# Optimization experiments

Measured on AMD Instinct MI355X. Metric: run time of the kernel, lower is better.

The kernel has to match this reference:

```python
import jax, jax.numpy as jnp
import numpy as np

B, L, H, S = 16, 2048, 1024, 32
P, N_ASP, N_RAT = 256, 8, 5


def _layernorm(x, scale, bias, eps=1e-5):
    mu = jnp.mean(x, axis=-1, keepdims=True)
    var = jnp.mean(jnp.square(x - mu), axis=-1, keepdims=True)
    return (x - mu) * jax.lax.rsqrt(var + eps) * scale + bias


def _bndl(x, ln_s, ln_b, W):
    # BnDropLin eval: LayerNorm -> (Dropout off) -> Linear(no bias)
    return _layernorm(x, ln_s, ln_b) @ W


def setup_inputs() -> dict:
    key = jax.random.key(0)
    ks = jax.random.split(key, 8)
    outputs = jax.random.normal(ks[0], (B, L, H), dtype=jnp.float32)
    mask = jnp.ones((B, L), dtype=jnp.float32)
    # p_index: binary sentence-boundary markers, exactly S per doc, min gap 2
    rng = np.random.default_rng(0)
    p = np.zeros((B, L), dtype=np.int32)
    for b in range(B):
        idx = np.sort(rng.choice(L // 2 - 1, size=S, replace=False)) * 2 + 1
        p[b, idx] = 1
    p_index = jnp.asarray(p)
    sc = 0.02
    params = dict(
        ln_a_s=jnp.ones((H,), jnp.float32), ln_a_b=jnp.zeros((H,), jnp.float32),
        W_a=jax.random.normal(ks[1], (H, P), jnp.float32) * sc,
        ln_s_s=jnp.ones((H,), jnp.float32), ln_s_b=jnp.zeros((H,), jnp.float32),
        W_s=jax.random.normal(ks[2], (H, P), jnp.float32) * sc,
        ln_asp_s=jnp.ones((P,), jnp.float32), ln_asp_b=jnp.zeros((P,), jnp.float32),
        W_asp=jax.random.normal(ks[3], (P, N_ASP + 1), jnp.float32) * sc,
        ln_se_s=jnp.ones((P,), jnp.float32), ln_se_b=jnp.zeros((P,), jnp.float32),
        W_se=jax.random.normal(ks[4], (P, N_RAT), jnp.float32) * sc,
    )
    return dict(outputs=outputs, mask=mask, p_index=p_index, n_sent=S, **params)


def _segment_means(proj, end, start):
    # proj: [B, L, P]; start/end: [B, S] token index ranges [start, end)
    c = jnp.concatenate([jnp.zeros_like(proj[:, :1]), jnp.cumsum(proj, axis=1)], axis=1)  # [B,L+1,P]
    s_end = jnp.take_along_axis(c, end[:, :, None], axis=1)
    s_beg = jnp.take_along_axis(c, start[:, :, None], axis=1)
    cnt = (end - start).astype(proj.dtype)[:, :, None]
    return (s_end - s_beg) / cnt  # [B, S, P]


def reference(outputs, mask, p_index, n_sent,
              ln_a_s, ln_a_b, W_a, ln_s_s, ln_s_b, W_s,
              ln_asp_s, ln_asp_b, W_asp, ln_se_s, ln_se_b, W_se):
    b, l, h = outputs.shape
    n_asp = W_asp.shape[1] - 1
    flat = outputs.reshape(-1, h)
    a_proj = jax.nn.gelu(_bndl(flat, ln_a_s, ln_a_b, W_a), approximate=False).reshape(b, l, -1)
    s_proj = jax.nn.gelu(_bndl(flat, ln_s_s, ln_s_b, W_s), approximate=False).reshape(b, l, -1)
    # sentence boundaries: positions of nonzeros (exactly n_sent per row)
    pos = jnp.where(p_index > 0, jnp.arange(l)[None, :], l)
    pi = jnp.sort(pos, axis=1)[:, :n_sent]                      # [B,S] boundary idx (exclusive end)
    start = jnp.concatenate([jnp.zeros_like(pi[:, :1]), pi[:, :-1] + 1], axis=1)
    a_sent = _segment_means(a_proj, pi, start)                  # [B,S,P]
    s_sent = _segment_means(s_proj, pi, start)                  # [B,S,P]
    a_flat = a_sent.reshape(b * n_sent, -1)
    s_flat = s_sent.reshape(b * n_sent, -1)
    aspect_dist = jax.nn.softmax(_bndl(a_flat, ln_asp_s, ln_asp_b, W_asp), axis=1)  # [N, n_asp+1]
    aw = aspect_dist[:, :n_asp]                                 # [N, n_asp]
    sent_bmm = aw[:, :, None] * s_flat[:, None, :]              # [N, n_asp, P]
    doc_sum = sent_bmm.reshape(b, n_sent, n_asp, -1).sum(axis=1)        # [B, n_asp, P]
    w_sum = aw.reshape(b, n_sent, n_asp).sum(axis=1)[:, :, None]        # [B, n_asp, 1]
    doc_emb = doc_sum / w_sum
    # shared sentiment head (ModuleList([m]*n_asp) aliases one module)
    result = _bndl(doc_emb, ln_se_s, ln_se_b, W_se)             # [B, n_asp, n_rat]
    aspect_doc = aspect_dist.reshape(b, n_sent, n_asp + 1)
    return (result, outputs, aspect_doc)
```

## Files before the change

### kernel.cpp

```cpp
#include <hip/hip_runtime.h>
#include <cstdint>
#include <cstddef>

#define B_   16
#define L_   2048
#define H_   1024
#define S_   32
#define P_   256
#define NASP 8
#define NRAT 5
#define M_   (B_*L_)
#define N_   (2*P_)

typedef unsigned short u16;
typedef __bf16 bf16;
typedef u16  u16x4  __attribute__((ext_vector_type(4)));
typedef u16  u16x8  __attribute__((ext_vector_type(8)));
typedef bf16 bf16x8 __attribute__((ext_vector_type(8)));
typedef float f32x4 __attribute__((ext_vector_type(4)));

__device__ __forceinline__ u16 f2b(float f){
  unsigned int u = __float_as_uint(f);
  u += 0x7FFFu + ((u >> 16) & 1u);
  return (u16)(u >> 16);
}
__device__ __forceinline__ float b2f(u16 v){
  return __uint_as_float(((unsigned int)v) << 16);
}

__device__ __forceinline__ void gload_lds16(const u16* g, u16* l){
  __builtin_amdgcn_global_load_lds(
      (const __attribute__((address_space(1))) unsigned int*)g,
      (__attribute__((address_space(3))) unsigned int*)l, 16, 0, 0);
}

__device__ __forceinline__ float2 block_reduce2(float a, float b){
  __shared__ float sh[8];
  #pragma unroll
  for (int o = 32; o > 0; o >>= 1){
    a += __shfl_down(a, o, 64);
    b += __shfl_down(b, o, 64);
  }
  int w = threadIdx.x >> 6;
  if ((threadIdx.x & 63) == 0){ sh[w] = a; sh[w + 4] = b; }
  __syncthreads();
  float2 r;
  r.x = sh[0] + sh[1] + sh[2] + sh[3];
  r.y = sh[4] + sh[5] + sh[6] + sh[7];
  __syncthreads();
  return r;
}

__global__ void fold_k(const float* __restrict__ Wa, const float* __restrict__ Ws,
                       const float* __restrict__ sa, const float* __restrict__ ba,
                       const float* __restrict__ ss, const float* __restrict__ bs,
                       u16* __restrict__ WcT, float* __restrict__ biasc){
  int n = blockIdx.x;
  const float* W; const float* sc; const float* bi; int col;
  if (n < P_){ W = Wa; sc = sa; bi = ba; col = n; }
  else       { W = Ws; sc = ss; bi = bs; col = n - P_; }
  float bacc = 0.f;
  #pragma unroll
  for (int i = 0; i < 4; ++i){
    int k = threadIdx.x + i * 256;
    float w = W[(size_t)k * P_ + col];
    WcT[(size_t)n * H_ + k] = f2b(w * sc[k]);
    bacc += w * bi[k];
  }
  float2 r = block_reduce2(bacc, 0.f);
  if (threadIdx.x == 0) biasc[n] = r.x;
}

__global__ void markers_k(const int* __restrict__ p_index, int* __restrict__ pi){
  int b = blockIdx.x;
  int lane = threadIdx.x;
  int cnt = 0;
  for (int c = 0; c < L_ / 64; ++c){
    int pos = c * 64 + lane;
    bool f = p_index[(size_t)b * L_ + pos] > 0;
    unsigned long long m = __ballot(f);
    int before = __popcll(m & ((1ull << lane) - 1ull));
    if (f){
      int idx = cnt + before;
      if (idx < S_) pi[b * S_ + idx] = pos;
    }
    cnt += __popcll(m);
  }
}

template<bool FUSE_ECHO>
__global__ void stats_xhat_k(const float* __restrict__ x, u16* __restrict__ xhat,
                             float4* __restrict__ echo){
  int row = blockIdx.x;
  int t = threadIdx.x;
  float4 v = ((const float4*)(x + (size_t)row * H_))[t];
  if (FUSE_ECHO) echo[(size_t)row * (H_ / 4) + t] = v;
  float s  = v.x + v.y + v.z + v.w;
  float ss = v.x*v.x + v.y*v.y + v.z*v.z + v.w*v.w;
  float2 r = block_reduce2(s, ss);
  float mean = r.x * (1.f / H_);
  float var  = fmaxf(r.y * (1.f / H_) - mean * mean, 0.f);
  float rstd = rsqrtf(var + 1e-5f);
  u16x4 o;
  o[0] = f2b((v.x - mean) * rstd);
  o[1] = f2b((v.y - mean) * rstd);
  o[2] = f2b((v.z - mean) * rstd);
  o[3] = f2b((v.w - mean) * rstd);
  ((u16x4*)(xhat + (size_t)row * H_))[t] = o;
}

__global__ __launch_bounds__(256) void gemm_k(const u16* __restrict__ xhat,
                                              const u16* __restrict__ WcT,
                                              const float* __restrict__ biasc,
                                              u16* __restrict__ proj){
  __shared__ __align__(16) u16 As[2 * 128 * 32];
  __shared__ __align__(16) u16 Bs[2 * 128 * 32];
  int t = threadIdx.x;
  unsigned int l = blockIdx.x;
  unsigned int xcd  = l & 7;
  unsigned int slot = l >> 3;
  int nbase = (int)(slot & 3) * 128;
  int mbase = (int)(xcd * 32 + (slot >> 2)) * 128;

  int w = t >> 6, lane = t & 63;
  int wr = w >> 1, wc = w & 1;
  int quad = lane >> 4, l15 = lane & 15;

  int g = (lane & 3) ^ ((lane >> 3) & 3);
  int r0 = (w * 2 + 0) * 16 + (lane >> 2);
  int r1 = (w * 2 + 1) * 16 + (lane >> 2);
  const u16* gA0 = xhat + (size_t)(mbase + r0) * H_ + g * 8;
  const u16* gA1 = xhat + (size_t)(mbase + r1) * H_ + g * 8;
  const u16* gB0 = WcT  + (size_t)(nbase + r0) * H_ + g * 8;
  const u16* gB1 = WcT  + (size_t)(nbase + r1) * H_ + g * 8;

  f32x4 acc[4][4] = {};

  auto stage = [&](int bb, int kk){
    u16* a = As + bb * 4096 + (w * 2) * 512;
    u16* b = Bs + bb * 4096 + (w * 2) * 512;
    gload_lds16(gA0 + kk, a);
    gload_lds16(gA1 + kk, a + 512);
    gload_lds16(gB0 + kk, b);
    gload_lds16(gB1 + kk, b + 512);
  };
  auto compute = [&](int bb){
    const u16* ab = As + bb * 4096;
    const u16* bb_ = Bs + bb * 4096;
    bf16x8 af[4], bfr[4];
    #pragma unroll
    for (int im = 0; im < 4; ++im){
      int R = wr * 64 + im * 16 + l15;
      int cq = quad ^ ((R >> 1) & 3);
      af[im] = *reinterpret_cast<const bf16x8*>(&ab[R * 32 + cq * 8]);
    }
    #pragma unroll
    for (int in = 0; in < 4; ++in){
      int R = wc * 64 + in * 16 + l15;
      int cq = quad ^ ((R >> 1) & 3);
      bfr[in] = *reinterpret_cast<const bf16x8*>(&bb_[R * 32 + cq * 8]);
    }
    #pragma unroll
    for (int im = 0; im < 4; ++im)
      #pragma unroll
      for (int in = 0; in < 4; ++in)
        acc[im][in] = __builtin_amdgcn_mfma_f32_16x16x32_bf16(af[im], bfr[in], acc[im][in], 0, 0, 0);
  };

  stage(0, 0);
  __syncthreads();
  int cur = 0;
  for (int step = 0; step < 31; ++step){
    stage(cur ^ 1, (step + 1) * 32);
    compute(cur);
    __syncthreads();
    cur ^= 1;
  }
  compute(cur);

  #pragma unroll
  for (int in = 0; in < 4; ++in){
    int col = nbase + wc * 64 + in * 16 + l15;
    float bv = biasc[col];
    #pragma unroll
    for (int im = 0; im < 4; ++im){
      #pragma unroll
      for (int r = 0; r < 4; ++r){
        int rowg = mbase + wr * 64 + im * 16 + quad * 4 + r;
        float vv = acc[im][in][r] + bv;
        float gl = 0.5f * vv * (1.0f + erff(vv * 0.70710678118654752f));
        proj[(size_t)rowg * N_ + col] = f2b(gl);
      }
    }
  }
}

__global__ __launch_bounds__(1024) void segmean_k(const u16* __restrict__ proj,
                                                  const int* __restrict__ pi,
                                                  float* __restrict__ sent){
  int b = blockIdx.x, j = blockIdx.y;
  int t = threadIdx.x;
  int rg   = t >> 6;
  int lane = t & 63;
  int end   = pi[b * S_ + j];
  int start = (j == 0) ? 0 : (pi[b * S_ + j - 1] + 1);
  end   = min(max(end, 0), L_);
  start = min(max(start, 0), end);
  int cnt = max(end - start, 1);
  float inv = 1.0f / (float)cnt;

  float s[8] = {};
  const u16* base = proj + ((size_t)b * L_ + start) * N_ + lane * 8;
  for (int r = rg; r < cnt; r += 16){
    u16x8 v = *reinterpret_cast<const u16x8*>(base + (size_t)r * N_);
    #pragma unroll
    for (int k = 0; k < 8; ++k) s[k] += b2f(v[k]);
  }

  __shared__ float sh[16][N_];
  #pragma unroll
  for (int k = 0; k < 8; ++k) sh[rg][lane * 8 + k] = s[k];
  __syncthreads();

  if (t < N_){
    float acc = 0.f;
    #pragma unroll
    for (int g = 0; g < 16; ++g) acc += sh[g][t];
    sent[((size_t)b * S_ + j) * N_ + t] = acc * inv;
  }
}

__global__ void aspect_k(const float* __restrict__ sent,
                         const float* __restrict__ lns, const float* __restrict__ lnb,
                         const float* __restrict__ Wasp,
                         float* __restrict__ out_adoc, float* __restrict__ aw){
  int sidx = blockIdx.x;
  int t = threadIdx.x;
  float a = sent[(size_t)sidx * N_ + t];
  float2 r = block_reduce2(a, a * a);
  float mean = r.x * (1.f / P_);
  float var  = fmaxf(r.y * (1.f / P_) - mean * mean, 0.f);
  float rstd = rsqrtf(var + 1e-5f);
  __shared__ float shv[P_];
  shv[t] = (a - mean) * rstd * lns[t] + lnb[t];
  __syncthreads();
  __shared__ float lg[NASP + 1];
  if (t < NASP + 1){
    float acc = 0.f;
    for (int p = 0; p < P_; ++p) acc += shv[p] * Wasp[p * (NASP + 1) + t];
    lg[t] = acc;
  }
  __syncthreads();
  __shared__ float pr[NASP + 1];
  if (t == 0){
    float m = lg[0];
    #pragma unroll
    for (int i = 1; i < NASP + 1; ++i) m = fmaxf(m, lg[i]);
    float s = 0.f;
    #pragma unroll
    for (int i = 0; i < NASP + 1; ++i){ float e = expf(lg[i] - m); pr[i] = e; s += e; }
    float is = 1.f / s;
    #pragma unroll
    for (int i = 0; i < NASP + 1; ++i) pr[i] *= is;
  }
  __syncthreads();
  if (t < NASP + 1) out_adoc[(size_t)sidx * (NASP + 1) + t] = pr[t];
  if (t < NASP)     aw[(size_t)sidx * NASP + t] = pr[t];
}

__global__ void result_k(const float* __restrict__ sent, const float* __restrict__ aw,
                         const float* __restrict__ lns, const float* __restrict__ lnb,
                         const float* __restrict__ Wse, float* __restrict__ out){
  int ba = blockIdx.x;
  int b = ba >> 3, a = ba & 7;
  int t = threadIdx.x;
  float acc = 0.f, wsum = 0.f;
  for (int s2 = 0; s2 < S_; ++s2){
    float w = aw[((size_t)(b * S_ + s2)) * NASP + a];
    acc  += w * sent[((size_t)(b * S_ + s2)) * N_ + P_ + t];
    wsum += w;
  }
  float d = acc / fmaxf(wsum, 1e-20f);
  float2 r = block_reduce2(d, d * d);
  float mean = r.x * (1.f / P_);
  float var  = fmaxf(r.y * (1.f / P_) - mean * mean, 0.f);
  float rstd = rsqrtf(var + 1e-5f);
  __shared__ float shv[P_];
  shv[t] = (d - mean) * rstd * lns[t] + lnb[t];
  __syncthreads();
  if (t < NRAT){
    float s = 0.f;
    for (int p = 0; p < P_; ++p) s += shv[p] * Wse[p * NRAT + t];
    out[(size_t)ba * NRAT + t] = s;
  }
}

__global__ void copy_k(const float4* __restrict__ src, float4* __restrict__ dst){
  size_t i = (size_t)blockIdx.x * 256 + threadIdx.x;
  dst[i] = src[i];
}

extern "C" void kernel_launch(void* const* d_in, const int* in_sizes, int n_in,
                              void* d_out, int out_size, void* d_ws, size_t ws_size,
                              hipStream_t stream) {
  const float* x        = (const float*)d_in[0];
  const int*   p_index  = (const int*)d_in[2];
  const float* ln_a_s   = (const float*)d_in[4];
  const float* ln_a_b   = (const float*)d_in[5];
  const float* W_a      = (const float*)d_in[6];
  const float* ln_s_s   = (const float*)d_in[7];
  const float* ln_s_b   = (const float*)d_in[8];
  const float* W_s      = (const float*)d_in[9];
  const float* ln_asp_s = (const float*)d_in[10];
  const float* ln_asp_b = (const float*)d_in[11];
  const float* W_asp    = (const float*)d_in[12];
  const float* ln_se_s  = (const float*)d_in[13];
  const float* ln_se_b  = (const float*)d_in[14];
  const float* W_se     = (const float*)d_in[15];

  float* out_result = (float*)d_out;
  float* out_echo   = out_result + 640;
  float* out_adoc   = out_echo + (size_t)M_ * H_;

  char* ws = (char*)d_ws;
  u16*   WcT   = (u16*)ws;   ws += (size_t)N_ * H_ * 2;
  float* biasc = (float*)ws; ws += (size_t)N_ * 4;
  int*   pi    = (int*)ws;   ws += (size_t)B_ * S_ * 4;
  float* sent  = (float*)ws; ws += (size_t)B_ * S_ * N_ * 4;
  float* aw    = (float*)ws; ws += (size_t)B_ * S_ * NASP * 4;

  size_t small_used = (size_t)(ws - (char*)d_ws);
  size_t big_need   = small_used + (size_t)M_ * N_ * 2 + (size_t)M_ * H_ * 2;
  bool   big_ws     = ws_size >= big_need;

  u16* proj; u16* xhat;
  if (big_ws){
    proj = (u16*)ws;
    xhat = proj + (size_t)M_ * N_;
  } else {
    proj = (u16*)out_echo;
    xhat = proj + (size_t)M_ * N_;
  }

  fold_k<<<N_, 256, 0, stream>>>(W_a, W_s, ln_a_s, ln_a_b, ln_s_s, ln_s_b, WcT, biasc);
  markers_k<<<B_, 64, 0, stream>>>(p_index, pi);
  if (big_ws)
    stats_xhat_k<true ><<<M_, 256, 0, stream>>>(x, xhat, (float4*)out_echo);
  else
    stats_xhat_k<false><<<M_, 256, 0, stream>>>(x, xhat, nullptr);
  gemm_k<<<1024, 256, 0, stream>>>(xhat, WcT, biasc, proj);
  segmean_k<<<dim3(B_, S_), 1024, 0, stream>>>(proj, pi, sent);
  aspect_k<<<B_ * S_, 256, 0, stream>>>(sent, ln_asp_s, ln_asp_b, W_asp, out_adoc, aw);
  result_k<<<B_ * NASP, 256, 0, stream>>>(sent, aw, ln_se_s, ln_se_b, W_se, out_result);
  if (!big_ws)
    copy_k<<<(M_ * H_ / 4) / 256, 256, 0, stream>>>((const float4*)x, (float4*)out_echo);
}
```

Measured before the change: 412.9 us.

## Replace double-buffered K=32 GEMM pipeline with single-buffered K=64 tiles

The GEMM main loop drops LDS double buffering with K=32 slices and instead loads a single 128x64 tile per iteration, guarded by two barriers, then runs two MFMA sub-steps over it. The LDS swizzle moves to an 8-way XOR on the row index to fit the 64-wide rows. This halves the number of loop iterations and barrier pairs per K, but global loads no longer overlap with MFMA compute inside a block, so latency hiding depends on other resident blocks.

```diff
diff --git a/kernel.cpp b/kernel.cpp
--- a/kernel.cpp
+++ b/kernel.cpp
@@ -113,8 +113,8 @@
                                               const u16* __restrict__ WcT,
                                               const float* __restrict__ biasc,
                                               u16* __restrict__ proj){
-  __shared__ __align__(16) u16 As[2 * 128 * 32];
-  __shared__ __align__(16) u16 Bs[2 * 128 * 32];
+  __shared__ __align__(16) u16 As[128 * 64];
+  __shared__ __align__(16) u16 Bs[128 * 64];
   int t = threadIdx.x;
   unsigned int l = blockIdx.x;
   unsigned int xcd  = l & 7;
@@ -126,57 +126,51 @@
   int wr = w >> 1, wc = w & 1;
   int quad = lane >> 4, l15 = lane & 15;
 
-  int g = (lane & 3) ^ ((lane >> 3) & 3);
-  int r0 = (w * 2 + 0) * 16 + (lane >> 2);
-  int r1 = (w * 2 + 1) * 16 + (lane >> 2);
-  const u16* gA0 = xhat + (size_t)(mbase + r0) * H_ + g * 8;
-  const u16* gA1 = xhat + (size_t)(mbase + r1) * H_ + g * 8;
-  const u16* gB0 = WcT  + (size_t)(nbase + r0) * H_ + g * 8;
-  const u16* gB1 = WcT  + (size_t)(nbase + r1) * H_ + g * 8;
+  int rin = lane >> 3;
+  int g = (lane & 7) ^ rin;
+  const u16* gA[4]; const u16* gB[4]; u16* lA[4]; u16* lB[4];
+  #pragma unroll
+  for (int i = 0; i < 4; ++i){
+    int r = w * 32 + i * 8 + rin;
+    gA[i] = xhat + (size_t)(mbase + r) * H_ + g * 8;
+    gB[i] = WcT  + (size_t)(nbase + r) * H_ + g * 8;
+    lA[i] = As + (w * 4 + i) * 512;
+    lB[i] = Bs + (w * 4 + i) * 512;
+  }
 
   f32x4 acc[4][4] = {};
 
-  auto stage = [&](int bb, int kk){
-    u16* a = As + bb * 4096 + (w * 2) * 512;
-    u16* b = Bs + bb * 4096 + (w * 2) * 512;
-    gload_lds16(gA0 + kk, a);
-    gload_lds16(gA1 + kk, a + 512);
-    gload_lds16(gB0 + kk, b);
-    gload_lds16(gB1 + kk, b + 512);
-  };
-  auto compute = [&](int bb){
-    const u16* ab = As + bb * 4096;
-    const u16* bb_ = Bs + bb * 4096;
-    bf16x8 af[4], bfr[4];
-    #pragma unroll
-    for (int im = 0; im < 4; ++im){
-      int R = wr * 64 + im * 16 + l15;
-      int cq = quad ^ ((R >> 1) & 3);
-      af[im] = *reinterpret_cast<const bf16x8*>(&ab[R * 32 + cq * 8]);
+  for (int kk = 0; kk < H_; kk += 64){
+    __syncthreads();
+    #pragma unroll
+    for (int i = 0; i < 4; ++i){
+      gload_lds16(gA[i] + kk, lA[i]);
+      gload_lds16(gB[i] + kk, lB[i]);
     }
-    #pragma unroll
-    for (int in = 0; in < 4; ++in){
-      int R = wc * 64 + in * 16 + l15;
-      int cq = quad ^ ((R >> 1) & 3);
-      bfr[in] = *reinterpret_cast<const bf16x8*>(&bb_[R * 32 + cq * 8]);
+    __syncthreads();
+
+    #pragma unroll
+    for (int s = 0; s < 2; ++s){
+      bf16x8 af[4], bfr[4];
+      #pragma unroll
+      for (int im = 0; im < 4; ++im){
+        int R = wr * 64 + im * 16 + l15;
+        int c = (s * 4 + quad) ^ (R & 7);
+        af[im] = *reinterpret_cast<const bf16x8*>(&As[R * 64 + c * 8]);
+      }
+      #pragma unroll
+      for (int in = 0; in < 4; ++in){
+        int R = wc * 64 + in * 16 + l15;
+        int c = (s * 4 + quad) ^ (R & 7);
+        bfr[in] = *reinterpret_cast<const bf16x8*>(&Bs[R * 64 + c * 8]);
+      }
+      #pragma unroll
+      for (int im = 0; im < 4; ++im)
+        #pragma unroll
+        for (int in = 0; in < 4; ++in)
+          acc[im][in] = __builtin_amdgcn_mfma_f32_16x16x32_bf16(af[im], bfr[in], acc[im][in], 0, 0, 0);
     }
-    #pragma unroll
-    for (int im = 0; im < 4; ++im)
-      #pragma unroll
-      for (int in = 0; in < 4; ++in)
-        acc[im][in] = __builtin_amdgcn_mfma_f32_16x16x32_bf16(af[im], bfr[in], acc[im][in], 0, 0, 0);
-  };
-
-  stage(0, 0);
-  __syncthreads();
-  int cur = 0;
-  for (int step = 0; step < 31; ++step){
-    stage(cur ^ 1, (step + 1) * 32);
-    compute(cur);
-    __syncthreads();
-    cur ^= 1;
-  }
-  compute(cur);
+  }
 
   #pragma unroll
   for (int in = 0; in < 4; ++in){
```

Result: faster. 400.5 us (-3.0%).
